# Performance work log

Measured on AMD Instinct MI355X. Metric: run time of the kernel, lower is better.

## Reference

```python
import jax, jax.numpy as jnp
import numpy as np

D = 128        # node_representation_size
V = 100000     # unique_internal_nodes (embedding vocab)
N = 20000      # nodes in the internal graph
E = 640000     # total neighbor (edge) entries


def setup_inputs() -> dict:
    key = jax.random.key(0)
    k1, k2, k3, k4, k5, k6 = jax.random.split(key, 6)
    node_ids = jax.random.randint(k1, (N,), 0, V)
    neighbor_ids = jax.random.randint(k2, (E,), 0, V)
    segment_ids = jnp.sort(jax.random.randint(k3, (E,), 0, N))
    xav = 1.0 / np.sqrt(D)  # xavier_normal std for square [D,D]
    W = jax.random.normal(k4, (D, D), dtype=jnp.float32) * xav
    M = jax.random.normal(k5, (D, D), dtype=jnp.float32) * xav
    emb = jax.random.normal(k6, (V, D), dtype=jnp.float32)
    return {"node_ids": node_ids, "neighbor_ids": neighbor_ids,
            "segment_ids": segment_ids, "W": W, "M": M, "emb": emb}


def reference(node_ids, neighbor_ids, segment_ids, W, M, emb):
    # Per node: s = relu(W @ e[node] + sum_{nbr} M @ e[nbr]); result = sum_nodes s
    self_term = emb[node_ids] @ W.T                       # [N, D]
    nb_msgs = emb[neighbor_ids] @ M.T                     # [E, D]
    nb_agg = jax.ops.segment_sum(nb_msgs, segment_ids, num_segments=N)  # [N, D]
    per_node = jax.nn.relu(self_term + nb_agg)            # [N, D]
    result = per_node.sum(axis=0)                         # [D]
    return jax.nn.softmax(result)[:, None]                # [D, 1], softmax over dim 0
```

## Files before the change

### kernel.cpp

```cpp
#include <hip/hip_runtime.h>

#define D 128
#define RS_STRIDE 64

typedef __attribute__((ext_vector_type(8))) short bf16x8;
typedef __attribute__((ext_vector_type(8))) unsigned short u16x8;
typedef __attribute__((ext_vector_type(4))) float f32x4;
typedef __attribute__((ext_vector_type(2))) float f32x2;

__device__ __forceinline__ unsigned short f2bf(float f) {
    unsigned u = __float_as_uint(f);
    unsigned r = (u + 0x7fffu + ((u >> 16) & 1u)) >> 16;
    return (unsigned short)r;
}
__device__ __forceinline__ float bf2f(unsigned short h) {
    return __uint_as_float(((unsigned)h) << 16);
}
__device__ __forceinline__ ushort4 pack4(float4 v) {
    ushort4 o; o.x = f2bf(v.x); o.y = f2bf(v.y); o.z = f2bf(v.z); o.w = f2bf(v.w);
    return o;
}
__device__ __forceinline__ void red3(float& x) {
    x += __shfl_xor(x, 8);
    x += __shfl_xor(x, 16);
    x += __shfl_xor(x, 32);
}
__device__ __forceinline__ void acc4(unsigned v, float* s) {
    f32x2 lo = __builtin_amdgcn_cvt_pk_f32_fp8(v, false);
    f32x2 hi = __builtin_amdgcn_cvt_pk_f32_fp8(v, true);
    s[0] += lo[0]; s[1] += lo[1]; s[2] += hi[0]; s[3] += hi[1];
}
__device__ __forceinline__ void acc16(uint4 v, float* s) {
    acc4(v.x, s); acc4(v.y, s + 4); acc4(v.z, s + 8); acc4(v.w, s + 12);
}
__device__ __forceinline__ int swz(int r, int s) {
    return r * D + ((s ^ (r & 7)) << 3);
}

__global__ void prep_kernel(const float* __restrict__ emb, const float* __restrict__ W,
                            const float* __restrict__ M, const int* __restrict__ seg,
                            unsigned char* __restrict__ emb8,
                            unsigned short* __restrict__ Wb, unsigned short* __restrict__ Mb,
                            float* __restrict__ rs, int* __restrict__ row_ptr,
                            int n4, int E, int N) {
    int i = blockIdx.x * blockDim.x + threadIdx.x;
    if (i < n4) {
        float4 v = ((const float4*)emb)[i];
        int p = __builtin_amdgcn_cvt_pk_fp8_f32(v.x, v.y, 0, false);
        p = __builtin_amdgcn_cvt_pk_fp8_f32(v.z, v.w, p, true);
        ((unsigned*)emb8)[i] = (unsigned)p;
    }
    if (i < 4096)       ((ushort4*)Wb)[i]        = pack4(((const float4*)W)[i]);
    else if (i < 8192)  ((ushort4*)Mb)[i - 4096] = pack4(((const float4*)M)[i - 4096]);
    if (i < D) rs[i * RS_STRIDE] = 0.0f;
    if (i < E) {
        int s = seg[i];
        if (i == 0) {
            for (int n = 0; n <= s; ++n) row_ptr[n] = 0;
        } else {
            int sp = seg[i - 1];
            for (int n = sp + 1; n <= s; ++n) row_ptr[n] = i;
        }
        if (i == E - 1) {
            for (int n = s + 1; n <= N; ++n) row_ptr[n] = E;
        }
    }
}

__global__ __launch_bounds__(256) void fused_kernel(
    const int* __restrict__ node_ids, const int* __restrict__ nbr,
    const int* __restrict__ row_ptr, const unsigned char* __restrict__ emb8,
    const unsigned short* __restrict__ Wb, const unsigned short* __restrict__ Mb,
    float* __restrict__ rs, int N) {
    __shared__ unsigned short xs[8 * D];
    __shared__ unsigned short as_[8 * D];

    int t = threadIdx.x;
    int w = t >> 6;
    int tt = t & 63;
    int g = blockIdx.x;

    {
        int c = tt & 7;
        int j = tt >> 3;
        for (int i = 0; i < 2; ++i) {
            int r = w * 2 + i;
            int n = g * 8 + r;
            bool valid = n < N;

            uint4 xv = make_uint4(0u, 0u, 0u, 0u);
            if (valid && j == 0)
                xv = *(const uint4*)(emb8 + (size_t)node_ids[n] * D + c * 16);

            float s[16];
#pragma unroll
            for (int k = 0; k < 16; ++k) s[k] = 0.f;

            int lo = valid ? row_ptr[n] : 0;
            int hi = valid ? row_ptr[n + 1] : 0;
            int e = lo + j;
            for (; e + 24 < hi; e += 32) {
                int i0 = nbr[e];
                int i1 = nbr[e + 8];
                int i2 = nbr[e + 16];
                int i3 = nbr[e + 24];
                uint4 a = *(const uint4*)(emb8 + (size_t)i0 * D + c * 16);
                uint4 b = *(const uint4*)(emb8 + (size_t)i1 * D + c * 16);
                uint4 d = *(const uint4*)(emb8 + (size_t)i2 * D + c * 16);
                uint4 f = *(const uint4*)(emb8 + (size_t)i3 * D + c * 16);
                acc16(a, s); acc16(b, s); acc16(d, s); acc16(f, s);
            }
            if (e + 8 < hi) {
                int i0 = nbr[e];
                int i1 = nbr[e + 8];
                uint4 a = *(const uint4*)(emb8 + (size_t)i0 * D + c * 16);
                uint4 b = *(const uint4*)(emb8 + (size_t)i1 * D + c * 16);
                acc16(a, s); acc16(b, s);
                e += 16;
            }
            if (e < hi) {
                uint4 a = *(const uint4*)(emb8 + (size_t)nbr[e] * D + c * 16);
                acc16(a, s);
            }
#pragma unroll
            for (int k = 0; k < 16; ++k) red3(s[k]);

            if (j == 0) {
                u16x8 o0, o1;
#pragma unroll
                for (int k = 0; k < 8; ++k) { o0[k] = f2bf(s[k]); o1[k] = f2bf(s[k + 8]); }
                *(u16x8*)&as_[swz(r, 2 * c)]     = o0;
                *(u16x8*)&as_[swz(r, 2 * c + 1)] = o1;

                float x[16];
#pragma unroll
                for (int k = 0; k < 16; ++k) x[k] = 0.f;
                acc16(xv, x);
                u16x8 p0, p1;
#pragma unroll
                for (int k = 0; k < 8; ++k) { p0[k] = f2bf(x[k]); p1[k] = f2bf(x[k + 8]); }
                *(u16x8*)&xs[swz(r, 2 * c)]     = p0;
                *(u16x8*)&xs[swz(r, 2 * c + 1)] = p1;
            }
        }
    }
    __syncthreads();

    int quad = tt >> 4, col = tt & 15;
    const bf16x8 zero8 = {0, 0, 0, 0, 0, 0, 0, 0};
    bf16x8 ax[4], aa[4];
#pragma unroll
    for (int ks = 0; ks < 4; ++ks) {
        if (col < 8) {
            ax[ks] = *(const bf16x8*)&xs[swz(col, ks * 4 + quad)];
            aa[ks] = *(const bf16x8*)&as_[swz(col, ks * 4 + quad)];
        } else {
            ax[ks] = zero8;
            aa[ks] = zero8;
        }
    }
#pragma unroll
    for (int p = 0; p < 2; ++p) {
        int dt = w + p * 4;
        int wrow = (dt * 16 + col) * D + quad * 8;
        f32x4 acc = {0.f, 0.f, 0.f, 0.f};
#pragma unroll
        for (int ks = 0; ks < 4; ++ks) {
            bf16x8 bw = *(const bf16x8*)(Wb + wrow + ks * 32);
            bf16x8 bm = *(const bf16x8*)(Mb + wrow + ks * 32);
            acc = __builtin_amdgcn_mfma_f32_16x16x32_bf16(ax[ks], bw, acc, 0, 0, 0);
            acc = __builtin_amdgcn_mfma_f32_16x16x32_bf16(aa[ks], bm, acc, 0, 0, 0);
        }
        float v = fmaxf(acc[0], 0.f) + fmaxf(acc[1], 0.f)
                + fmaxf(acc[2], 0.f) + fmaxf(acc[3], 0.f);
        v += __shfl_xor(v, 16);
        v += __shfl_xor(v, 32);
        if (tt < 16) atomicAdd(&rs[(dt * 16 + col) * RS_STRIDE], v);
    }
}

__global__ void agg_f32_kernel(const int* __restrict__ nbr, const int* __restrict__ row_ptr,
                               const float* __restrict__ emb,
                               unsigned short* __restrict__ aggb, int N) {
    int n = blockIdx.x * 4 + (threadIdx.x >> 6);
    if (n >= N) return;
    int tt = threadIdx.x & 63;
    int c = tt & 7;
    int j = tt >> 3;

    int lo = row_ptr[n], hi = row_ptr[n + 1];

    float4 s0 = make_float4(0.f, 0.f, 0.f, 0.f);
    float4 s1 = make_float4(0.f, 0.f, 0.f, 0.f);
    float4 s2 = make_float4(0.f, 0.f, 0.f, 0.f);
    float4 s3 = make_float4(0.f, 0.f, 0.f, 0.f);
    for (int e = lo + j; e < hi; e += 8) {
        const float4* r = (const float4*)&emb[(size_t)nbr[e] * D];
        float4 v0 = r[c], v1 = r[c + 8], v2 = r[c + 16], v3 = r[c + 24];
        s0.x += v0.x; s0.y += v0.y; s0.z += v0.z; s0.w += v0.w;
        s1.x += v1.x; s1.y += v1.y; s1.z += v1.z; s1.w += v1.w;
        s2.x += v2.x; s2.y += v2.y; s2.z += v2.z; s2.w += v2.w;
        s3.x += v3.x; s3.y += v3.y; s3.z += v3.z; s3.w += v3.w;
    }
    red3(s0.x); red3(s0.y); red3(s0.z); red3(s0.w);
    red3(s1.x); red3(s1.y); red3(s1.z); red3(s1.w);
    red3(s2.x); red3(s2.y); red3(s2.z); red3(s2.w);
    red3(s3.x); red3(s3.y); red3(s3.z); red3(s3.w);
    if (j == 0) {
        ushort4* o = (ushort4*)(aggb + (size_t)n * D);
        o[c]      = pack4(s0);
        o[c + 8]  = pack4(s1);
        o[c + 16] = pack4(s2);
        o[c + 24] = pack4(s3);
    }
}

__global__ __launch_bounds__(256) void matvec_f32_kernel(
    const int* __restrict__ node_ids, const float* __restrict__ emb,
    const unsigned short* __restrict__ aggb,
    const unsigned short* __restrict__ Wb, const unsigned short* __restrict__ Mb,
    float* __restrict__ rs, int N, int ngroups, int nstripes) {
    int t = threadIdx.x;
    int wid = blockIdx.x * 4 + (t >> 6);
    int l = t & 63;
    int quad = l >> 4, col = l & 15;
    int dt = wid & 7;
    int stripe = wid >> 3;

    bf16x8 bw[4], bm[4];
    int wrow = (dt * 16 + col) * D;
#pragma unroll
    for (int ks = 0; ks < 4; ++ks) {
        int off = wrow + ks * 32 + quad * 8;
        bw[ks] = *(const bf16x8*)(Wb + off);
        bm[ks] = *(const bf16x8*)(Mb + off);
    }

    const bf16x8 zero8 = {0, 0, 0, 0, 0, 0, 0, 0};
    float vsum = 0.f;

    for (int grp = stripe; grp < ngroups; grp += nstripes) {
        int node = grp * 16 + col;
        bool valid = node < N;
        int nid = valid ? node_ids[node] : 0;
        const unsigned short* ar = aggb + (size_t)node * D + quad * 8;

        f32x4 acc = {0.f, 0.f, 0.f, 0.f};
#pragma unroll
        for (int ks = 0; ks < 4; ++ks) {
            bf16x8 ax;
            if (valid) {
                const float4* xf = (const float4*)(emb +
                                   (size_t)nid * D + quad * 8 + ks * 32);
                ushort4 p0 = pack4(xf[0]);
                ushort4 p1 = pack4(xf[1]);
                ax[0] = (short)p0.x; ax[1] = (short)p0.y;
                ax[2] = (short)p0.z; ax[3] = (short)p0.w;
                ax[4] = (short)p1.x; ax[5] = (short)p1.y;
                ax[6] = (short)p1.z; ax[7] = (short)p1.w;
            } else ax = zero8;
            bf16x8 aa = valid ? *(const bf16x8*)(ar + ks * 32) : zero8;
            acc = __builtin_amdgcn_mfma_f32_16x16x32_bf16(ax, bw[ks], acc, 0, 0, 0);
            acc = __builtin_amdgcn_mfma_f32_16x16x32_bf16(aa, bm[ks], acc, 0, 0, 0);
        }
        vsum += fmaxf(acc[0], 0.f) + fmaxf(acc[1], 0.f)
              + fmaxf(acc[2], 0.f) + fmaxf(acc[3], 0.f);
    }

    vsum += __shfl_xor(vsum, 16);
    vsum += __shfl_xor(vsum, 32);
    if (l < 16) atomicAdd(&rs[(dt * 16 + col) * RS_STRIDE], vsum);
}

__global__ void softmax_kernel(const float* __restrict__ rs, float* __restrict__ out) {
    int t = threadIdx.x;
    float v0 = rs[t * RS_STRIDE];
    float v1 = rs[(t + 64) * RS_STRIDE];
    float m = fmaxf(v0, v1);
    for (int o = 32; o > 0; o >>= 1) m = fmaxf(m, __shfl_xor(m, o));
    float e0 = expf(v0 - m);
    float e1 = expf(v1 - m);
    float s = e0 + e1;
    for (int o = 32; o > 0; o >>= 1) s += __shfl_xor(s, o);
    float inv = 1.0f / s;
    out[t] = e0 * inv;
    out[t + 64] = e1 * inv;
}

extern "C" void kernel_launch(void* const* d_in, const int* in_sizes, int n_in,
                              void* d_out, int out_size, void* d_ws, size_t ws_size,
                              hipStream_t stream) {
    const int*   node_ids = (const int*)d_in[0];
    const int*   nbr      = (const int*)d_in[1];
    const int*   seg      = (const int*)d_in[2];
    const float* W        = (const float*)d_in[3];
    const float* M        = (const float*)d_in[4];
    const float* emb      = (const float*)d_in[5];
    float* out = (float*)d_out;

    int N = in_sizes[0];
    int E = in_sizes[1];
    long long VD = in_sizes[5];
    int ngroups8 = (N + 7) / 8;

    unsigned short* aggb = (unsigned short*)d_ws;
    unsigned short* Wb   = aggb + (size_t)N * D;
    unsigned short* Mb   = Wb + D * D;
    float* rs            = (float*)(Mb + D * D);
    int* row_ptr         = (int*)(rs + (size_t)D * RS_STRIDE);
    unsigned char* emb8  = (unsigned char*)(row_ptr + (N + 1));

    size_t need_fp8 = (size_t)((char*)emb8 - (char*)d_ws) + (size_t)VD;
    bool use_fp8 = ws_size >= need_fp8;
    int n4 = use_fp8 ? (int)(VD / 4) : 0;
    int cvt_n = (n4 > 8192 ? n4 : 8192);
    int prep_n = (cvt_n > E ? cvt_n : E);

    prep_kernel<<<(prep_n + 255) / 256, 256, 0, stream>>>(emb, M ? W : W, M, seg, emb8, Wb, Mb,
                                                          rs, row_ptr, n4, E, N);
    if (use_fp8) {
        fused_kernel<<<ngroups8, 256, 0, stream>>>(node_ids, nbr, row_ptr, emb8,
                                                   Wb, Mb, rs, N);
    } else {
        int ngroups  = (N + 15) / 16;
        int nstripes = (ngroups + 1) / 2;
        agg_f32_kernel<<<(N + 3) / 4, 256, 0, stream>>>(nbr, row_ptr, emb, aggb, N);
        matvec_f32_kernel<<<2 * nstripes, 256, 0, stream>>>(node_ids, emb, aggb, Wb, Mb,
                                                            rs, N, ngroups, nstripes);
    }
    softmax_kernel<<<1, 64, 0, stream>>>(rs, out);
}
```

Baseline: 158.9 us.

## Widen fused block to 16 nodes and fold softmax into last-block epilogue

The fused kernel now runs 512 threads over 16 nodes per block, so the MFMA A tile is fully used instead of half zero-padded. Each wave computes one 16-column output tile, which halves W/M loads per node and halves the atomics on rs. The separate softmax launch is removed: a global done counter picks the last finishing block, and that block computes the softmax. This adds a threadfence plus an extra atomic per block, and halves the number of blocks, which may reduce latency hiding on the gather phase.

```diff
diff --git a/kernel.cpp b/kernel.cpp
--- a/kernel.cpp
+++ b/kernel.cpp
@@ -12,9 +12,6 @@
     unsigned u = __float_as_uint(f);
     unsigned r = (u + 0x7fffu + ((u >> 16) & 1u)) >> 16;
     return (unsigned short)r;
-}
-__device__ __forceinline__ float bf2f(unsigned short h) {
-    return __uint_as_float(((unsigned)h) << 16);
 }
 __device__ __forceinline__ ushort4 pack4(float4 v) {
     ushort4 o; o.x = f2bf(v.x); o.y = f2bf(v.y); o.z = f2bf(v.z); o.w = f2bf(v.w);
@@ -42,7 +39,7 @@
                             unsigned char* __restrict__ emb8,
                             unsigned short* __restrict__ Wb, unsigned short* __restrict__ Mb,
                             float* __restrict__ rs, int* __restrict__ row_ptr,
-                            int n4, int E, int N) {
+                            unsigned* __restrict__ done, int n4, int E, int N) {
     int i = blockIdx.x * blockDim.x + threadIdx.x;
     if (i < n4) {
         float4 v = ((const float4*)emb)[i];
@@ -53,6 +50,7 @@
     if (i < 4096)       ((ushort4*)Wb)[i]        = pack4(((const float4*)W)[i]);
     else if (i < 8192)  ((ushort4*)Mb)[i - 4096] = pack4(((const float4*)M)[i - 4096]);
     if (i < D) rs[i * RS_STRIDE] = 0.0f;
+    if (i == 0) *done = 0u;
     if (i < E) {
         int s = seg[i];
         if (i == 0) {
@@ -67,13 +65,15 @@
     }
 }
 
-__global__ __launch_bounds__(256) void fused_kernel(
+__global__ __launch_bounds__(512) void fused_kernel(
     const int* __restrict__ node_ids, const int* __restrict__ nbr,
     const int* __restrict__ row_ptr, const unsigned char* __restrict__ emb8,
     const unsigned short* __restrict__ Wb, const unsigned short* __restrict__ Mb,
-    float* __restrict__ rs, int N) {
-    __shared__ unsigned short xs[8 * D];
-    __shared__ unsigned short as_[8 * D];
+    float* __restrict__ rs, unsigned* __restrict__ done,
+    float* __restrict__ out, int N) {
+    __shared__ unsigned short xs[16 * D];
+    __shared__ unsigned short as_[16 * D];
+    __shared__ int last;
 
     int t = threadIdx.x;
     int w = t >> 6;
@@ -85,7 +85,7 @@
         int j = tt >> 3;
         for (int i = 0; i < 2; ++i) {
             int r = w * 2 + i;
-            int n = g * 8 + r;
+            int n = g * 16 + r;
             bool valid = n < N;
 
             uint4 xv = make_uint4(0u, 0u, 0u, 0u);
@@ -147,35 +147,43 @@
     __syncthreads();
 
     int quad = tt >> 4, col = tt & 15;
-    const bf16x8 zero8 = {0, 0, 0, 0, 0, 0, 0, 0};
     bf16x8 ax[4], aa[4];
 #pragma unroll
     for (int ks = 0; ks < 4; ++ks) {
-        if (col < 8) {
-            ax[ks] = *(const bf16x8*)&xs[swz(col, ks * 4 + quad)];
-            aa[ks] = *(const bf16x8*)&as_[swz(col, ks * 4 + quad)];
-        } else {
-            ax[ks] = zero8;
-            aa[ks] = zero8;
-        }
-    }
-#pragma unroll
-    for (int p = 0; p < 2; ++p) {
-        int dt = w + p * 4;
-        int wrow = (dt * 16 + col) * D + quad * 8;
-        f32x4 acc = {0.f, 0.f, 0.f, 0.f};
-#pragma unroll
-        for (int ks = 0; ks < 4; ++ks) {
-            bf16x8 bw = *(const bf16x8*)(Wb + wrow + ks * 32);
-            bf16x8 bm = *(const bf16x8*)(Mb + wrow + ks * 32);
-            acc = __builtin_amdgcn_mfma_f32_16x16x32_bf16(ax[ks], bw, acc, 0, 0, 0);
-            acc = __builtin_amdgcn_mfma_f32_16x16x32_bf16(aa[ks], bm, acc, 0, 0, 0);
-        }
-        float v = fmaxf(acc[0], 0.f) + fmaxf(acc[1], 0.f)
-                + fmaxf(acc[2], 0.f) + fmaxf(acc[3], 0.f);
-        v += __shfl_xor(v, 16);
-        v += __shfl_xor(v, 32);
-        if (tt < 16) atomicAdd(&rs[(dt * 16 + col) * RS_STRIDE], v);
+        ax[ks] = *(const bf16x8*)&xs[swz(col, ks * 4 + quad)];
+        aa[ks] = *(const bf16x8*)&as_[swz(col, ks * 4 + quad)];
+    }
+    int wrow = (w * 16 + col) * D + quad * 8;
+    f32x4 acc = {0.f, 0.f, 0.f, 0.f};
+#pragma unroll
+    for (int ks = 0; ks < 4; ++ks) {
+        bf16x8 bw = *(const bf16x8*)(Wb + wrow + ks * 32);
+        bf16x8 bm = *(const bf16x8*)(Mb + wrow + ks * 32);
+        acc = __builtin_amdgcn_mfma_f32_16x16x32_bf16(ax[ks], bw, acc, 0, 0, 0);
+        acc = __builtin_amdgcn_mfma_f32_16x16x32_bf16(aa[ks], bm, acc, 0, 0, 0);
+    }
+    float v = fmaxf(acc[0], 0.f) + fmaxf(acc[1], 0.f)
+            + fmaxf(acc[2], 0.f) + fmaxf(acc[3], 0.f);
+    v += __shfl_xor(v, 16);
+    v += __shfl_xor(v, 32);
+    if (tt < 16) atomicAdd(&rs[(w * 16 + col) * RS_STRIDE], v);
+
+    __threadfence();
+    __syncthreads();
+    if (t == 0) last = (atomicAdd(done, 1u) == gridDim.x - 1) ? 1 : 0;
+    __syncthreads();
+    if (last && t < 64) {
+        float v0 = atomicAdd(&rs[t * RS_STRIDE], 0.0f);
+        float v1 = atomicAdd(&rs[(t + 64) * RS_STRIDE], 0.0f);
+        float m = fmaxf(v0, v1);
+        for (int o = 32; o > 0; o >>= 1) m = fmaxf(m, __shfl_xor(m, o));
+        float e0 = expf(v0 - m);
+        float e1 = expf(v1 - m);
+        float su = e0 + e1;
+        for (int o = 32; o > 0; o >>= 1) su += __shfl_xor(su, o);
+        float inv = 1.0f / su;
+        out[t] = e0 * inv;
+        out[t + 64] = e1 * inv;
     }
 }
 
@@ -301,7 +309,7 @@
     int N = in_sizes[0];
     int E = in_sizes[1];
     long long VD = in_sizes[5];
-    int ngroups8 = (N + 7) / 8;
+    int ngroups  = (N + 15) / 16;
 
     unsigned short* aggb = (unsigned short*)d_ws;
     unsigned short* Wb   = aggb + (size_t)N * D;
@@ -309,24 +317,24 @@
     float* rs            = (float*)(Mb + D * D);
     int* row_ptr         = (int*)(rs + (size_t)D * RS_STRIDE);
     unsigned char* emb8  = (unsigned char*)(row_ptr + (N + 1));
-
-    size_t need_fp8 = (size_t)((char*)emb8 - (char*)d_ws) + (size_t)VD;
+    unsigned* done       = (unsigned*)(emb8 + VD);
+
+    size_t need_fp8 = (size_t)((char*)emb8 - (char*)d_ws) + (size_t)VD + 16;
     bool use_fp8 = ws_size >= need_fp8;
     int n4 = use_fp8 ? (int)(VD / 4) : 0;
     int cvt_n = (n4 > 8192 ? n4 : 8192);
     int prep_n = (cvt_n > E ? cvt_n : E);
 
-    prep_kernel<<<(prep_n + 255) / 256, 256, 0, stream>>>(emb, M ? W : W, M, seg, emb8, Wb, Mb,
-                                                          rs, row_ptr, n4, E, N);
+    prep_kernel<<<(prep_n + 255) / 256, 256, 0, stream>>>(emb, W, M, seg, emb8, Wb, Mb,
+                                                          rs, row_ptr, done, n4, E, N);
     if (use_fp8) {
-        fused_kernel<<<ngroups8, 256, 0, stream>>>(node_ids, nbr, row_ptr, emb8,
-                                                   Wb, Mb, rs, N);
+        fused_kernel<<<ngroups, 512, 0, stream>>>(node_ids, nbr, row_ptr, emb8,
+                                                  Wb, Mb, rs, done, out, N);
     } else {
-        int ngroups  = (N + 15) / 16;
         int nstripes = (ngroups + 1) / 2;
         agg_f32_kernel<<<(N + 3) / 4, 256, 0, stream>>>(nbr, row_ptr, emb, aggb, N);
         matvec_f32_kernel<<<2 * nstripes, 256, 0, stream>>>(node_ids, emb, aggb, Wb, Mb,
                                                             rs, N, ngroups, nstripes);
-    }
-    softmax_kernel<<<1, 64, 0, stream>>>(rs, out);
-}
+        softmax_kernel<<<1, 64, 0, stream>>>(rs, out);
+    }
+}
```

After: 311.2 us. +95.9%, slower.
